# Kernel tuning notes

Measured on AMD Instinct MI355X. Metric: run time of the kernel, lower is better.

The kernel has to match this reference:

```python
import jax, jax.numpy as jnp
import numpy as np

F_DIM, HID, H, DQ, DV = 1024, 4096, 16, 64, 64
EPS = 1e-6

def layer_norm(x, w, b):
    mu = jnp.mean(x, axis=-1, keepdims=True)
    var = jnp.mean(jnp.square(x - mu), axis=-1, keepdims=True)
    return (x - mu) * jax.lax.rsqrt(var + EPS) * w + b

def setup_inputs() -> dict:
    key = jax.random.key(0)
    ks = jax.random.split(key, 8)
    s = 0.02
    return {
        'x': jax.random.normal(ks[0], (4, 2048, F_DIM), dtype=jnp.float32),
        'ln1_w': jnp.ones((F_DIM,), jnp.float32),
        'ln1_b': jnp.zeros((F_DIM,), jnp.float32),
        'wq_w': jax.random.normal(ks[1], (H * DQ, F_DIM), jnp.float32) * s,
        'wq_b': jnp.zeros((H * DQ,), jnp.float32),
        'wk_w': jax.random.normal(ks[2], (H * DQ, F_DIM), jnp.float32) * s,
        'wk_b': jnp.zeros((H * DQ,), jnp.float32),
        'wv_w': jax.random.normal(ks[3], (H * DV, F_DIM), jnp.float32) * s,
        'wv_b': jnp.zeros((H * DV,), jnp.float32),
        'fc_w': jax.random.normal(ks[4], (F_DIM, H * DV), jnp.float32) * s,
        'fc_b': jnp.zeros((F_DIM,), jnp.float32),
        'ln2_w': jnp.ones((F_DIM,), jnp.float32),
        'ln2_b': jnp.zeros((F_DIM,), jnp.float32),
        'fc1_w': jax.random.normal(ks[5], (HID, F_DIM), jnp.float32) * s,
        'fc1_b': jnp.zeros((HID,), jnp.float32),
        'fc2_w': jax.random.normal(ks[6], (F_DIM, HID), jnp.float32) * s,
        'fc2_b': jnp.zeros((F_DIM,), jnp.float32),
    }

def reference(x, ln1_w, ln1_b, wq_w, wq_b, wk_w, wk_b, wv_w, wv_b,
              fc_w, fc_b, ln2_w, ln2_b, fc1_w, fc1_b, fc2_w, fc2_b):
    B, S, _ = x.shape
    # --- pre-LN multi-head self-attention ---
    h = layer_norm(x, ln1_w, ln1_b)
    q = (h @ wq_w.T + wq_b).reshape(B, S, H, DQ).transpose(0, 2, 1, 3)  # [B,H,S,dq]
    k = (h @ wk_w.T + wk_b).reshape(B, S, H, DQ).transpose(0, 2, 1, 3)
    v = (h @ wv_w.T + wv_b).reshape(B, S, H, DV).transpose(0, 2, 1, 3)
    attn = jax.nn.softmax(jnp.einsum('bhqd,bhkd->bhqk', q, k) / jnp.sqrt(jnp.float32(DQ)), axis=-1)
    out = jnp.einsum('bhqk,bhkd->bhqd', attn, v).transpose(0, 2, 1, 3).reshape(B, S, H * DV)
    x = x + (out @ fc_w.T + fc_b)
    # --- pre-LN residual MLP ---
    h2 = layer_norm(x, ln2_w, ln2_b)
    ff = jax.nn.relu(h2 @ fc1_w.T + fc1_b) @ fc2_w.T + fc2_b
    return x + ff
```

## Files before the change

### kernel.cpp

```cpp
#include <hip/hip_runtime.h>

#define F_DIMC 1024
#define HIDC   4096
#define NH     16
#define SEQ    2048
#define BATCH  4
#define ROWS   (BATCH * SEQ)
#define MEG    (1u << 20)
#define QSCALE 0.18033688011112042f

typedef unsigned short u16t;
typedef __attribute__((ext_vector_type(8))) short short8;
typedef __attribute__((ext_vector_type(4))) float floatx4;
typedef __attribute__((address_space(1))) void gvoid_t;
typedef __attribute__((address_space(3))) void lvoid_t;
#define ASYNC16(g, l) __builtin_amdgcn_global_load_lds((gvoid_t*)(g), (lvoid_t*)(l), 16, 0, 0)

__device__ __forceinline__ u16t f2bf(float f) {
    union { float f; unsigned u; } v; v.f = f;
    unsigned r = v.u + 0x7fffu + ((v.u >> 16) & 1u);
    return (u16t)(r >> 16);
}

__global__ __launch_bounds__(256) void ln_kernel(const float* __restrict__ x,
                                                 const float* __restrict__ w,
                                                 const float* __restrict__ b,
                                                 u16t* __restrict__ out) {
    const int row = blockIdx.x;
    const int t = threadIdx.x;
    const float* xp = x + (size_t)row * F_DIMC;

    float4 v = *(const float4*)(xp + t * 4);
    float s  = v.x + v.y + v.z + v.w;
    float ss = v.x * v.x + v.y * v.y + v.z * v.z + v.w * v.w;
    for (int off = 32; off; off >>= 1) {
        s  += __shfl_down(s, off);
        ss += __shfl_down(ss, off);
    }
    __shared__ float red[8];
    const int wid = t >> 6, lid = t & 63;
    if (lid == 0) { red[wid] = s; red[4 + wid] = ss; }
    __syncthreads();
    if (t == 0) {
        float S  = red[0] + red[1] + red[2] + red[3];
        float SS = red[4] + red[5] + red[6] + red[7];
        float mu  = S * (1.0f / F_DIMC);
        float var = SS * (1.0f / F_DIMC) - mu * mu;
        red[0] = mu;
        red[1] = rsqrtf(var + 1e-6f);
    }
    __syncthreads();
    const float mu = red[0], rs = red[1];

    float4 wv = *(const float4*)(w + t * 4);
    float4 bv = *(const float4*)(b + t * 4);
    ushort4 o = make_ushort4(f2bf((v.x - mu) * rs * wv.x + bv.x),
                             f2bf((v.y - mu) * rs * wv.y + bv.y),
                             f2bf((v.z - mu) * rs * wv.z + bv.z),
                             f2bf((v.w - mu) * rs * wv.w + bv.w));
    *(ushort4*)(out + (size_t)row * F_DIMC + t * 4) = o;
}

__global__ __launch_bounds__(256) void wconv_kernel(const float* __restrict__ w0,
        const float* __restrict__ w1, const float* __restrict__ w2,
        const float* __restrict__ w3, const float* __restrict__ w4,
        const float* __restrict__ w5, u16t* __restrict__ dst) {
    const size_t e = ((size_t)blockIdx.x * 256 + threadIdx.x) * 4;
    const float* src; size_t off;
    if      (e < 1 * MEG) { src = w0; off = e; }
    else if (e < 2 * MEG) { src = w1; off = e - 1 * MEG; }
    else if (e < 3 * MEG) { src = w2; off = e - 2 * MEG; }
    else if (e < 4 * MEG) { src = w3; off = e - 3 * MEG; }
    else if (e < 8 * MEG) { src = w4; off = e - 4 * MEG; }
    else                  { src = w5; off = e - 8 * MEG; }
    float4 f = *(const float4*)(src + off);
    *(ushort4*)(dst + e) = make_ushort4(f2bf(f.x), f2bf(f.y), f2bf(f.z), f2bf(f.w));
}

#define GEMM_PROLOGUE_AND_LOOP(Aq, Wq, Kdim)                                   \
    __shared__ u16t As[128 * 32] __attribute__((aligned(16)));                 \
    __shared__ u16t Ws[128 * 32] __attribute__((aligned(16)));                 \
    const int t = threadIdx.x;                                                 \
    const int lane = t & 63;                                                   \
    const int wave = t >> 6;                                                   \
    const int wm = wave >> 1, wn = wave & 1;                                   \
    const int m0 = blockIdx.y * 128, n0 = blockIdx.x * 128;                    \
    const int b0 = t, b1 = t + 256;                                            \
    const int r0 = b0 >> 2, r1 = b1 >> 2;                                      \
    const int q0_ = (b0 & 3) ^ (r0 & 3) ^ ((r0 >> 2) & 1);                     \
    const int q1_ = (b1 & 3) ^ (r1 & 3) ^ ((r1 >> 2) & 1);                     \
    const u16t* Ag0 = (Aq) + (size_t)(m0 + r0) * (Kdim) + q0_ * 8;             \
    const u16t* Ag1 = (Aq) + (size_t)(m0 + r1) * (Kdim) + q1_ * 8;             \
    const u16t* Wg0 = (Wq) + (size_t)(n0 + r0) * (Kdim) + q0_ * 8;             \
    const u16t* Wg1 = (Wq) + (size_t)(n0 + r1) * (Kdim) + q1_ * 8;             \
    u16t* Al0 = As + b0 * 8;  u16t* Al1 = As + b1 * 8;                         \
    u16t* Wl0 = Ws + b0 * 8;  u16t* Wl1 = Ws + b1 * 8;                         \
    const int fm = lane & 15, fq = lane >> 4;                                  \
    const int swz = fq ^ (fm & 3) ^ ((fm >> 2) & 1);                           \
    const u16t* Afp = As + ((wm * 64 + fm) * 32 + swz * 8);                    \
    const u16t* Wfp = Ws + ((wn * 64 + fm) * 32 + swz * 8);                    \
    floatx4 acc[4][4] = {};                                                    \
    for (int k0 = 0; k0 < (Kdim); k0 += 32) {                                  \
        ASYNC16(Ag0, Al0); ASYNC16(Ag1, Al1);                                  \
        ASYNC16(Wg0, Wl0); ASYNC16(Wg1, Wl1);                                  \
        Ag0 += 32; Ag1 += 32; Wg0 += 32; Wg1 += 32;                            \
        __syncthreads();                                                       \
        short8 fa[4], fb[4];                                                   \
        _Pragma("unroll")                                                      \
        for (int i = 0; i < 4; ++i) {                                          \
            fa[i] = *(const short8*)(Afp + i * 16 * 32);                       \
            fb[i] = *(const short8*)(Wfp + i * 16 * 32);                       \
        }                                                                      \
        _Pragma("unroll")                                                      \
        for (int mi = 0; mi < 4; ++mi)                                         \
            _Pragma("unroll")                                                  \
            for (int ni = 0; ni < 4; ++ni)                                     \
                acc[mi][ni] = __builtin_amdgcn_mfma_f32_16x16x32_bf16(         \
                    fa[mi], fb[ni], acc[mi][ni], 0, 0, 0);                     \
        __syncthreads();                                                       \
    }

template <bool RELU, bool RES, bool BF16OUT>
__global__ __launch_bounds__(256) void gemm_mfma(const u16t* __restrict__ A,
                                                 const u16t* __restrict__ W,
                                                 const float* __restrict__ bias,
                                                 const float* res, void* Cout,
                                                 int N, int K) {
    GEMM_PROLOGUE_AND_LOOP(A, W, K)
    float bl[4];
#pragma unroll
    for (int ni = 0; ni < 4; ++ni) bl[ni] = bias[n0 + wn * 64 + ni * 16 + fm];
#pragma unroll
    for (int mi = 0; mi < 4; ++mi) {
#pragma unroll
        for (int ni = 0; ni < 4; ++ni) {
            const int col = n0 + wn * 64 + ni * 16 + fm;
#pragma unroll
            for (int r = 0; r < 4; ++r) {
                const int row = m0 + wm * 64 + mi * 16 + fq * 4 + r;
                const size_t off = (size_t)row * N + col;
                float c = acc[mi][ni][r] + bl[ni];
                if (RELU) c = fmaxf(c, 0.0f);
                if (RES)  c += res[off];
                if (BF16OUT) ((u16t*)Cout)[off] = f2bf(c);
                else         ((float*)Cout)[off] = c;
            }
        }
    }
}

__global__ __launch_bounds__(256) void gemm_qkv(const u16t* __restrict__ A,
        const u16t* __restrict__ W,
        const float* __restrict__ wq_b, const float* __restrict__ wk_b,
        const float* __restrict__ wv_b,
        u16t* __restrict__ qb, u16t* __restrict__ kb, u16t* __restrict__ vtb) {
    GEMM_PROLOGUE_AND_LOOP(A, W, F_DIMC)
    const int which = n0 >> 10;
    const int nb = n0 & 1023;
    const float* bias = which == 0 ? wq_b : which == 1 ? wk_b : wv_b;
    float bl[4];
#pragma unroll
    for (int ni = 0; ni < 4; ++ni) bl[ni] = bias[nb + wn * 64 + ni * 16 + fm];

    if (which == 2) {
#pragma unroll
        for (int mi = 0; mi < 4; ++mi)
#pragma unroll
            for (int ni = 0; ni < 4; ++ni) {
                const int col = nb + wn * 64 + ni * 16 + fm;
                const int row0 = m0 + wm * 64 + mi * 16 + fq * 4;
                ushort4 pk = make_ushort4(f2bf(acc[mi][ni][0] + bl[ni]),
                                          f2bf(acc[mi][ni][1] + bl[ni]),
                                          f2bf(acc[mi][ni][2] + bl[ni]),
                                          f2bf(acc[mi][ni][3] + bl[ni]));
                *(ushort4*)(vtb + (size_t)col * ROWS + row0) = pk;
            }
    } else {
        u16t* dst = (which == 0) ? qb : kb;
        const float sc = (which == 0) ? QSCALE : 1.0f;
#pragma unroll
        for (int mi = 0; mi < 4; ++mi)
#pragma unroll
            for (int ni = 0; ni < 4; ++ni) {
                const int col = nb + wn * 64 + ni * 16 + fm;
#pragma unroll
                for (int r = 0; r < 4; ++r) {
                    const int row = m0 + wm * 64 + mi * 16 + fq * 4 + r;
                    dst[(size_t)row * F_DIMC + col] = f2bf((acc[mi][ni][r] + bl[ni]) * sc);
                }
            }
    }
}

__global__ __launch_bounds__(256) void attn_mfma(const u16t* __restrict__ qb,
        const u16t* __restrict__ kbuf, const u16t* __restrict__ vtb,
        u16t* __restrict__ ab) {
    __shared__ u16t Kt[2][64 * 64] __attribute__((aligned(16)));
    __shared__ u16t Vs[2][64 * 64] __attribute__((aligned(16)));
    __shared__ u16t QP[128 * 64] __attribute__((aligned(16)));

    const int t = threadIdx.x;
    const int lane = t & 63;
    const int wave = t >> 6;
    const int l15 = lane & 15, q4 = lane >> 4;
    const int q0 = blockIdx.x * 128;
    const int bh = blockIdx.y;
    const int b = bh >> 4, hh = bh & 15;

#pragma unroll
    for (int c = 0; c < 4; ++c) {
        const int beta = c * 256 + t;
        const int r = beta >> 3, o = (beta & 7) ^ (r & 7);
        ASYNC16(qb + (size_t)(b * SEQ + q0 + r) * F_DIMC + hh * 64 + o * 8,
                QP + beta * 8);
    }
    const u16t* kg = kbuf + (size_t)(b * SEQ) * F_DIMC + hh * 64;
    const u16t* vg = vtb + (size_t)(hh * 64) * ROWS + b * SEQ;
#pragma unroll
    for (int c = 0; c < 2; ++c) {
        const int beta = c * 256 + t;
        const int r = beta >> 3, o = (beta & 7) ^ (r & 7);
        ASYNC16(kg + (size_t)r * F_DIMC + o * 8, Kt[0] + beta * 8);
        ASYNC16(vg + (size_t)r * ROWS + o * 8, Vs[0] + beta * 8);
    }
    __syncthreads();

    short8 fqr[2][2];
#pragma unroll
    for (int mt = 0; mt < 2; ++mt)
#pragma unroll
        for (int ks = 0; ks < 2; ++ks) {
            const int m = wave * 32 + mt * 16 + l15;
            const int oct = ks * 4 + q4;
            fqr[mt][ks] = *(const short8*)(QP + (m * 8 + (oct ^ (m & 7))) * 8);
        }

    floatx4 oacc[2][4] = {};
    float lsum[2] = {0.0f, 0.0f};

    for (int it = 0; it < SEQ / 64; ++it) {
        if (it + 1 < SEQ / 64) {
            const int kt1 = (it + 1) * 64;
            u16t* kd = Kt[(it + 1) & 1];
            u16t* vd = Vs[(it + 1) & 1];
#pragma unroll
            for (int c = 0; c < 2; ++c) {
                const int beta = c * 256 + t;
                const int r = beta >> 3, o = (beta & 7) ^ (r & 7);
                ASYNC16(kg + (size_t)(kt1 + r) * F_DIMC + o * 8, kd + beta * 8);
                ASYNC16(vg + (size_t)r * ROWS + kt1 + o * 8, vd + beta * 8);
            }
        }
        const u16t* kcur = Kt[it & 1];
        const u16t* vcur = Vs[it & 1];

        short8 fk[4][2];
#pragma unroll
        for (int nt = 0; nt < 4; ++nt)
#pragma unroll
            for (int ks = 0; ks < 2; ++ks) {
                const int kr = nt * 16 + l15;
                const int oct = ks * 4 + q4;
                fk[nt][ks] = *(const short8*)(kcur + (kr * 8 + (oct ^ (kr & 7))) * 8);
            }
        floatx4 st[2][4] = {};
#pragma unroll
        for (int mt = 0; mt < 2; ++mt)
#pragma unroll
            for (int nt = 0; nt < 4; ++nt) {
                st[mt][nt] = __builtin_amdgcn_mfma_f32_16x16x32_bf16(
                    fk[nt][0], fqr[mt][0], st[mt][nt], 0, 0, 0);
                st[mt][nt] = __builtin_amdgcn_mfma_f32_16x16x32_bf16(
                    fk[nt][1], fqr[mt][1], st[mt][nt], 0, 0, 0);
            }

#pragma unroll
        for (int mt = 0; mt < 2; ++mt)
#pragma unroll
            for (int nt = 0; nt < 4; ++nt) {
                ushort4 pk;
                float p0 = exp2f(st[mt][nt][0]);
                float p1 = exp2f(st[mt][nt][1]);
                float p2 = exp2f(st[mt][nt][2]);
                float p3 = exp2f(st[mt][nt][3]);
                lsum[mt] += (p0 + p1) + (p2 + p3);
                pk.x = f2bf(p0); pk.y = f2bf(p1); pk.z = f2bf(p2); pk.w = f2bf(p3);
                const int m = wave * 32 + mt * 16 + l15;
                const int logb = nt * 2 + (q4 >> 1);
                *(ushort4*)(QP + (m * 8 + (logb ^ (m & 7))) * 8 + (q4 & 1) * 4) = pk;
            }

        short8 fp[2][2], fv[4][2];
#pragma unroll
        for (int mt = 0; mt < 2; ++mt)
#pragma unroll
            for (int ks = 0; ks < 2; ++ks) {
                const int m = wave * 32 + mt * 16 + l15;
                const int oct = ks * 4 + q4;
                fp[mt][ks] = *(const short8*)(QP + (m * 8 + (oct ^ (m & 7))) * 8);
            }
#pragma unroll
        for (int nd = 0; nd < 4; ++nd)
#pragma unroll
            for (int ks = 0; ks < 2; ++ks) {
                const int d = nd * 16 + l15;
                const int oct = ks * 4 + q4;
                fv[nd][ks] = *(const short8*)(vcur + (d * 8 + (oct ^ (d & 7))) * 8);
            }
#pragma unroll
        for (int mt = 0; mt < 2; ++mt)
#pragma unroll
            for (int nd = 0; nd < 4; ++nd) {
                oacc[mt][nd] = __builtin_amdgcn_mfma_f32_16x16x32_bf16(
                    fp[mt][0], fv[nd][0], oacc[mt][nd], 0, 0, 0);
                oacc[mt][nd] = __builtin_amdgcn_mfma_f32_16x16x32_bf16(
                    fp[mt][1], fv[nd][1], oacc[mt][nd], 0, 0, 0);
            }
        __syncthreads();
    }

    float rinv[2][4];
#pragma unroll
    for (int mt = 0; mt < 2; ++mt) {
        float l = lsum[mt];
        l += __shfl_xor(l, 16);
        l += __shfl_xor(l, 32);
#pragma unroll
        for (int r = 0; r < 4; ++r)
            rinv[mt][r] = 1.0f / __shfl(l, q4 * 4 + r);
    }
#pragma unroll
    for (int mt = 0; mt < 2; ++mt)
#pragma unroll
        for (int nd = 0; nd < 4; ++nd)
#pragma unroll
            for (int r = 0; r < 4; ++r) {
                const int row = b * SEQ + q0 + wave * 32 + mt * 16 + q4 * 4 + r;
                const int col = hh * 64 + nd * 16 + l15;
                ab[(size_t)row * F_DIMC + col] = f2bf(oacc[mt][nd][r] * rinv[mt][r]);
            }
}

extern "C" void kernel_launch(void* const* d_in, const int* in_sizes, int n_in,
                              void* d_out, int out_size, void* d_ws, size_t ws_size,
                              hipStream_t stream) {
    const float* x     = (const float*)d_in[0];
    const float* ln1_w = (const float*)d_in[1];
    const float* ln1_b = (const float*)d_in[2];
    const float* wq_w  = (const float*)d_in[3];
    const float* wq_b  = (const float*)d_in[4];
    const float* wk_w  = (const float*)d_in[5];
    const float* wk_b  = (const float*)d_in[6];
    const float* wv_w  = (const float*)d_in[7];
    const float* wv_b  = (const float*)d_in[8];
    const float* fc_w  = (const float*)d_in[9];
    const float* fc_b  = (const float*)d_in[10];
    const float* ln2_w = (const float*)d_in[11];
    const float* ln2_b = (const float*)d_in[12];
    const float* fc1_w = (const float*)d_in[13];
    const float* fc1_b = (const float*)d_in[14];
    const float* fc2_w = (const float*)d_in[15];
    const float* fc2_b = (const float*)d_in[16];

    float* out = (float*)d_out;
    u16t*  ws  = (u16t*)d_ws;

    u16t* wbuf = ws;
    u16t* bwqkv = wbuf;
    u16t* bwfc = wbuf + 3 * MEG;
    u16t* bwf1 = wbuf + 4 * MEG;
    u16t* bwf2 = wbuf + 8 * MEG;
    u16t* h    = wbuf + 12 * MEG;
    u16t* qb   = h + 8 * MEG;
    u16t* kb   = qb + 8 * MEG;
    u16t* vtb  = kb + 8 * MEG;
    u16t* ab   = vtb + 8 * MEG;
    u16t* ff   = qb;

    const dim3 blk(256);
    const dim3 gF(F_DIMC / 128, ROWS / 128);
    const dim3 gQKV(3072 / 128, ROWS / 128);
    const dim3 gH(HIDC / 128, ROWS / 128);

    wconv_kernel<<<12 * MEG / 1024, blk, 0, stream>>>(wq_w, wk_w, wv_w, fc_w, fc1_w, fc2_w, wbuf);
    ln_kernel<<<ROWS, blk, 0, stream>>>(x, ln1_w, ln1_b, h);
    gemm_qkv<<<gQKV, blk, 0, stream>>>(h, bwqkv, wq_b, wk_b, wv_b, qb, kb, vtb);
    attn_mfma<<<dim3(SEQ / 128, BATCH * NH), blk, 0, stream>>>(qb, kb, vtb, ab);
    gemm_mfma<false, true, false><<<gF, blk, 0, stream>>>(ab, bwfc, fc_b, x, out, F_DIMC, F_DIMC);
    ln_kernel<<<ROWS, blk, 0, stream>>>(out, ln2_w, ln2_b, h);
    gemm_mfma<true, false, true><<<gH, blk, 0, stream>>>(h, bwf1, fc1_b, nullptr, ff, HIDC, F_DIMC);
    gemm_mfma<false, true, false><<<gF, blk, 0, stream>>>(ff, bwf2, fc2_b, out, out, F_DIMC, HIDC);
}
```

Measured before the change: 612.3 us.

## Restructure attention loop: single V buffer, MFMA row sums, fast exp and packing

The attention kernel moves from a double-buffered V tile to a single V buffer that is reloaded after the PV MFMAs. An extra barrier is added, and launch bounds are set for 4 blocks per CU, which frees LDS and raises occupancy. Softmax row sums are now computed by an MFMA against a vector of bf16 ones, replacing the scalar adds and cross-lane shuffles. The code also uses the hardware exp2 builtin and packs bf16 with a perm truncation instead of round-to-nearest. The costs are an extra __syncthreads per iteration, exposed V load latency, and truncation instead of rounding in the P values.

```diff
diff --git a/kernel.cpp b/kernel.cpp
--- a/kernel.cpp
+++ b/kernel.cpp
@@ -16,10 +16,19 @@
 typedef __attribute__((address_space(3))) void lvoid_t;
 #define ASYNC16(g, l) __builtin_amdgcn_global_load_lds((gvoid_t*)(g), (lvoid_t*)(l), 16, 0, 0)
 
+#if __has_builtin(__builtin_amdgcn_exp2f)
+#define EXP2(x) __builtin_amdgcn_exp2f(x)
+#else
+#define EXP2(x) exp2f(x)
+#endif
+
 __device__ __forceinline__ u16t f2bf(float f) {
     union { float f; unsigned u; } v; v.f = f;
     unsigned r = v.u + 0x7fffu + ((v.u >> 16) & 1u);
     return (u16t)(r >> 16);
+}
+__device__ __forceinline__ unsigned fasu(float f) {
+    union { float f; unsigned u; } v; v.f = f; return v.u;
 }
 
 __global__ __launch_bounds__(256) void ln_kernel(const float* __restrict__ x,
@@ -192,11 +201,11 @@
     }
 }
 
-__global__ __launch_bounds__(256) void attn_mfma(const u16t* __restrict__ qb,
+__global__ __launch_bounds__(256, 4) void attn_mfma(const u16t* __restrict__ qb,
         const u16t* __restrict__ kbuf, const u16t* __restrict__ vtb,
         u16t* __restrict__ ab) {
     __shared__ u16t Kt[2][64 * 64] __attribute__((aligned(16)));
-    __shared__ u16t Vs[2][64 * 64] __attribute__((aligned(16)));
+    __shared__ u16t Vs[64 * 64] __attribute__((aligned(16)));
     __shared__ u16t QP[128 * 64] __attribute__((aligned(16)));
 
     const int t = threadIdx.x;
@@ -216,13 +225,20 @@
     }
     const u16t* kg = kbuf + (size_t)(b * SEQ) * F_DIMC + hh * 64;
     const u16t* vg = vtb + (size_t)(hh * 64) * ROWS + b * SEQ;
-#pragma unroll
-    for (int c = 0; c < 2; ++c) {
-        const int beta = c * 256 + t;
-        const int r = beta >> 3, o = (beta & 7) ^ (r & 7);
-        ASYNC16(kg + (size_t)r * F_DIMC + o * 8, Kt[0] + beta * 8);
-        ASYNC16(vg + (size_t)r * ROWS + o * 8, Vs[0] + beta * 8);
-    }
+
+    const int sb0 = t, sb1 = t + 256;
+    const int sr0 = sb0 >> 3, so0 = (sb0 & 7) ^ (sr0 & 7);
+    const int sr1 = sb1 >> 3, so1 = (sb1 & 7) ^ (sr1 & 7);
+    const u16t* kp0 = kg + (size_t)sr0 * F_DIMC + so0 * 8;
+    const u16t* kp1 = kg + (size_t)sr1 * F_DIMC + so1 * 8;
+    const u16t* vp0 = vg + (size_t)sr0 * ROWS + so0 * 8;
+    const u16t* vp1 = vg + (size_t)sr1 * ROWS + so1 * 8;
+
+    ASYNC16(kp0, Kt[0] + sb0 * 8);
+    ASYNC16(kp1, Kt[0] + sb1 * 8);
+    ASYNC16(vp0, Vs + sb0 * 8);
+    ASYNC16(vp1, Vs + sb1 * 8);
+    kp0 += 64 * F_DIMC; kp1 += 64 * F_DIMC; vp0 += 64; vp1 += 64;
     __syncthreads();
 
     short8 fqr[2][2];
@@ -235,24 +251,21 @@
             fqr[mt][ks] = *(const short8*)(QP + (m * 8 + (oct ^ (m & 7))) * 8);
         }
 
+    short8 ones;
+#pragma unroll
+    for (int i = 0; i < 8; ++i) ones[i] = (short)0x3F80;
+
     floatx4 oacc[2][4] = {};
-    float lsum[2] = {0.0f, 0.0f};
+    floatx4 lacc[2] = {};
 
     for (int it = 0; it < SEQ / 64; ++it) {
         if (it + 1 < SEQ / 64) {
-            const int kt1 = (it + 1) * 64;
             u16t* kd = Kt[(it + 1) & 1];
-            u16t* vd = Vs[(it + 1) & 1];
-#pragma unroll
-            for (int c = 0; c < 2; ++c) {
-                const int beta = c * 256 + t;
-                const int r = beta >> 3, o = (beta & 7) ^ (r & 7);
-                ASYNC16(kg + (size_t)(kt1 + r) * F_DIMC + o * 8, kd + beta * 8);
-                ASYNC16(vg + (size_t)r * ROWS + kt1 + o * 8, vd + beta * 8);
-            }
+            ASYNC16(kp0, kd + sb0 * 8);
+            ASYNC16(kp1, kd + sb1 * 8);
+            kp0 += 64 * F_DIMC; kp1 += 64 * F_DIMC;
         }
         const u16t* kcur = Kt[it & 1];
-        const u16t* vcur = Vs[it & 1];
 
         short8 fk[4][2];
 #pragma unroll
@@ -278,17 +291,19 @@
         for (int mt = 0; mt < 2; ++mt)
 #pragma unroll
             for (int nt = 0; nt < 4; ++nt) {
-                ushort4 pk;
-                float p0 = exp2f(st[mt][nt][0]);
-                float p1 = exp2f(st[mt][nt][1]);
-                float p2 = exp2f(st[mt][nt][2]);
-                float p3 = exp2f(st[mt][nt][3]);
-                lsum[mt] += (p0 + p1) + (p2 + p3);
-                pk.x = f2bf(p0); pk.y = f2bf(p1); pk.z = f2bf(p2); pk.w = f2bf(p3);
+                const float p0 = EXP2(st[mt][nt][0]);
+                const float p1 = EXP2(st[mt][nt][1]);
+                const float p2 = EXP2(st[mt][nt][2]);
+                const float p3 = EXP2(st[mt][nt][3]);
+                const unsigned lo = __builtin_amdgcn_perm(fasu(p1), fasu(p0), 0x07060302u);
+                const unsigned hi = __builtin_amdgcn_perm(fasu(p3), fasu(p2), 0x07060302u);
                 const int m = wave * 32 + mt * 16 + l15;
                 const int logb = nt * 2 + (q4 >> 1);
-                *(ushort4*)(QP + (m * 8 + (logb ^ (m & 7))) * 8 + (q4 & 1) * 4) = pk;
-            }
+                *(uint2*)(QP + (m * 8 + (logb ^ (m & 7))) * 8 + (q4 & 1) * 4) =
+                    make_uint2(lo, hi);
+            }
+
+        __syncthreads();
 
         short8 fp[2][2], fv[4][2];
 #pragma unroll
@@ -305,10 +320,10 @@
             for (int ks = 0; ks < 2; ++ks) {
                 const int d = nd * 16 + l15;
                 const int oct = ks * 4 + q4;
-                fv[nd][ks] = *(const short8*)(vcur + (d * 8 + (oct ^ (d & 7))) * 8);
-            }
-#pragma unroll
-        for (int mt = 0; mt < 2; ++mt)
+                fv[nd][ks] = *(const short8*)(Vs + (d * 8 + (oct ^ (d & 7))) * 8);
+            }
+#pragma unroll
+        for (int mt = 0; mt < 2; ++mt) {
 #pragma unroll
             for (int nd = 0; nd < 4; ++nd) {
                 oacc[mt][nd] = __builtin_amdgcn_mfma_f32_16x16x32_bf16(
@@ -316,29 +331,34 @@
                 oacc[mt][nd] = __builtin_amdgcn_mfma_f32_16x16x32_bf16(
                     fp[mt][1], fv[nd][1], oacc[mt][nd], 0, 0, 0);
             }
+            lacc[mt] = __builtin_amdgcn_mfma_f32_16x16x32_bf16(
+                fp[mt][0], ones, lacc[mt], 0, 0, 0);
+            lacc[mt] = __builtin_amdgcn_mfma_f32_16x16x32_bf16(
+                fp[mt][1], ones, lacc[mt], 0, 0, 0);
+        }
+
         __syncthreads();
-    }
-
-    float rinv[2][4];
+        if (it + 1 < SEQ / 64) {
+            ASYNC16(vp0, Vs + sb0 * 8);
+            ASYNC16(vp1, Vs + sb1 * 8);
+            vp0 += 64; vp1 += 64;
+        }
+    }
+
 #pragma unroll
     for (int mt = 0; mt < 2; ++mt) {
-        float l = lsum[mt];
-        l += __shfl_xor(l, 16);
-        l += __shfl_xor(l, 32);
-#pragma unroll
-        for (int r = 0; r < 4; ++r)
-            rinv[mt][r] = 1.0f / __shfl(l, q4 * 4 + r);
-    }
-#pragma unroll
-    for (int mt = 0; mt < 2; ++mt)
+        floatx4 rinv;
+#pragma unroll
+        for (int r = 0; r < 4; ++r) rinv[r] = 1.0f / lacc[mt][r];
 #pragma unroll
         for (int nd = 0; nd < 4; ++nd)
 #pragma unroll
             for (int r = 0; r < 4; ++r) {
                 const int row = b * SEQ + q0 + wave * 32 + mt * 16 + q4 * 4 + r;
                 const int col = hh * 64 + nd * 16 + l15;
-                ab[(size_t)row * F_DIMC + col] = f2bf(oacc[mt][nd][r] * rinv[mt][r]);
-            }
+                ab[(size_t)row * F_DIMC + col] = f2bf(oacc[mt][nd][r] * rinv[r]);
+            }
+    }
 }
 
 extern "C" void kernel_launch(void* const* d_in, const int* in_sizes, int n_in,
```

Measured after the change: 559.4 us. 1.09x faster.
